# Performance work log

Hardware: AMD Instinct MI355X
Metric: run time of the kernel (lower is better)

The kernel has to match this reference:

```python
import jax, jax.numpy as jnp
import numpy as np

N_NODES = 100000
N_EDGES = 1600000
D_IN = 128
D_HID = 128
D_OUT = 1


def setup_inputs() -> dict:
    key = jax.random.key(0)
    ks = jax.random.split(key, 8)
    x = jax.random.normal(ks[0], (N_NODES, D_IN), dtype=jnp.float32)
    edge_index = jax.random.randint(ks[1], (2, N_EDGES), 0, N_NODES, dtype=jnp.int64)
    s1 = 1.0 / np.sqrt(D_IN)
    s2 = 1.0 / np.sqrt(D_HID)
    W1 = jax.random.uniform(ks[2], (D_IN, D_HID), jnp.float32, -s1, s1)
    b1 = jnp.zeros((D_HID,), jnp.float32)
    W2 = jax.random.uniform(ks[3], (D_HID, D_HID), jnp.float32, -s2, s2)
    b2 = jnp.zeros((D_HID,), jnp.float32)
    Wl = jax.random.uniform(ks[4], (D_HID, D_OUT), jnp.float32, -s2, s2)
    bl = jax.random.uniform(ks[5], (D_OUT,), jnp.float32, -s2, s2)
    return {"x": x, "edge_index": edge_index, "W1": W1, "b1": b1,
            "W2": W2, "b2": b2, "Wl": Wl, "bl": bl}


def _gcn_norm(edge_index, num_nodes):
    # Add self-loops, compute symmetric normalization 1/sqrt(deg_s * deg_d).
    loops = jnp.arange(num_nodes, dtype=edge_index.dtype)
    src = jnp.concatenate([edge_index[0], loops])
    dst = jnp.concatenate([edge_index[1], loops])
    deg = jax.ops.segment_sum(jnp.ones_like(dst, dtype=jnp.float32), dst,
                              num_segments=num_nodes)
    dinv = jnp.where(deg > 0, jax.lax.rsqrt(deg), 0.0)
    norm = dinv[src] * dinv[dst]  # [E + N]
    return src, dst, norm


def _gcn_conv(h, W, b, src, dst, norm, num_nodes):
    h = h @ W                                  # [N, d_out]
    msg = h[src] * norm[:, None]               # [E+N, d_out] gather
    out = jax.ops.segment_sum(msg, dst, num_segments=num_nodes)  # scatter-add
    return out + b


def reference(x, edge_index, W1, b1, W2, b2, Wl, bl):
    num_nodes = x.shape[0]
    src, dst, norm = _gcn_norm(edge_index, num_nodes)
    h = jax.nn.relu(_gcn_conv(x, W1, b1, src, dst, norm, num_nodes))
    # dropout is identity in eval mode
    h = jax.nn.relu(_gcn_conv(h, W2, b2, src, dst, norm, num_nodes))
    return h @ Wl + bl
```

## Files before the change

### kernel.cpp

```cpp
#include <hip/hip_runtime.h>

#define DHID 128
#define BCAP 10240
#define PCHUNK 4096

typedef _Float16 h4 __attribute__((ext_vector_type(4)));
typedef _Float16 h8 __attribute__((ext_vector_type(8)));
typedef _Float16 f16x8 __attribute__((ext_vector_type(8)));
typedef float    f32x4 __attribute__((ext_vector_type(4)));

__global__ __launch_bounds__(256) void k_partition(const int* __restrict__ ei, int E, int nbuck,
                                                   int* __restrict__ bucket_cursor,
                                                   unsigned* __restrict__ packed) {
    __shared__ unsigned sdata[PCHUNK];
    __shared__ int lcnt[256], lbase[256], loff[256], lcur[256], sscan[256];
    int t = threadIdx.x;
    int e0 = blockIdx.x * PCHUNK;
    lcnt[t] = 0;
    __syncthreads();

    for (int i = t; i < PCHUNK; i += 256) {
        int e = e0 + i;
        if (e < E) {
            int d = ei[E + e];
            atomicAdd(&lcnt[d >> 9], 1);
        }
    }
    __syncthreads();

    int c = lcnt[t];
    sscan[t] = c;
    __syncthreads();
    for (int off = 1; off < 256; off <<= 1) {
        int v = (t >= off) ? sscan[t - off] : 0;
        __syncthreads();
        sscan[t] += v;
        __syncthreads();
    }
    loff[t] = sscan[t] - c;
    if (t < nbuck && c > 0) lbase[t] = atomicAdd(&bucket_cursor[t], c);
    lcur[t] = sscan[t] - c;
    __syncthreads();

    for (int i = t; i < PCHUNK; i += 256) {
        int e = e0 + i;
        if (e < E) {
            int s = ei[e];
            int d = ei[E + e];
            int b = d >> 9;
            int pos = atomicAdd(&lcur[b], 1);
            sdata[pos] = ((unsigned)(d & 511) << 17) | (unsigned)s;
        }
    }
    __syncthreads();

    int wid = t >> 6, lane = t & 63;
    for (int b = wid; b < nbuck; b += 4) {
        int cb = lcnt[b];
        if (cb == 0) continue;
        int gbase = b * BCAP + lbase[b];
        int sbase = loff[b];
        for (int k = lane; k < cb; k += 64) packed[gbase + k] = sdata[sbase + k];
    }
}

__global__ __launch_bounds__(256) void k_p2a(const unsigned* __restrict__ packed,
                                             const int* __restrict__ bucket_cursor,
                                             int* __restrict__ cnt, int N) {
    __shared__ int c512[512];
    int t = threadIdx.x, b = blockIdx.x;
    c512[t] = 0; c512[t + 256] = 0;
    __syncthreads();
    int m = bucket_cursor[b];
    const unsigned* pb = packed + (size_t)b * BCAP;
    for (int i = t; i < m; i += 256) atomicAdd(&c512[pb[i] >> 17], 1);
    __syncthreads();
    int base = b << 9;
#pragma unroll
    for (int j = 0; j < 2; ++j) {
        int node = base + t + j * 256;
        if (node < N) cnt[node] = c512[t + j * 256];
    }
}

__global__ void k_dinv(const int* __restrict__ cnt, float* __restrict__ dinv, int N) {
    int i = blockIdx.x * 256 + threadIdx.x;
    if (i < N) dinv[i] = rsqrtf((float)(cnt[i] + 1));
}

__global__ void k_reduce(const int* __restrict__ cnt, int* __restrict__ partial, int N) {
    __shared__ int s[256];
    int t = threadIdx.x;
    int i = blockIdx.x * 256 + t;
    s[t] = (i < N) ? cnt[i] : 0;
    __syncthreads();
    for (int st = 128; st > 0; st >>= 1) {
        if (t < st) s[t] += s[t + st];
        __syncthreads();
    }
    if (t == 0) partial[blockIdx.x] = s[0];
}

__global__ void k_scan_partials(const int* __restrict__ partial, int* __restrict__ blockoff, int NB) {
    __shared__ int s[1024];
    int t = threadIdx.x;
    s[t] = (t < NB) ? partial[t] : 0;
    __syncthreads();
    for (int off = 1; off < 1024; off <<= 1) {
        int v = (t >= off) ? s[t - off] : 0;
        __syncthreads();
        s[t] += v;
        __syncthreads();
    }
    if (t < NB) blockoff[t] = (t == 0) ? 0 : s[t - 1];
}

__global__ void k_scan_block(const int* __restrict__ cnt, const int* __restrict__ blockoff,
                             int* __restrict__ row_ptr, int N, int E) {
    __shared__ int s[256];
    int t = threadIdx.x;
    int i = blockIdx.x * 256 + t;
    int c = (i < N) ? cnt[i] : 0;
    s[t] = c;
    __syncthreads();
    for (int off = 1; off < 256; off <<= 1) {
        int v = (t >= off) ? s[t - off] : 0;
        __syncthreads();
        s[t] += v;
        __syncthreads();
    }
    if (i < N) row_ptr[i] = blockoff[blockIdx.x] + s[t] - c;
    if (i == 0) row_ptr[N] = E;
}

__global__ __launch_bounds__(256) void k_p2b(const unsigned* __restrict__ packed,
                                             const int* __restrict__ bucket_cursor,
                                             const int* __restrict__ row_ptr,
                                             int* __restrict__ csr, int N) {
    __shared__ int c512[512], cur512[512], sscan[256];
    int t = threadIdx.x, b = blockIdx.x;
    c512[t] = 0; c512[t + 256] = 0;
    __syncthreads();
    int m = bucket_cursor[b];
    const unsigned* pb = packed + (size_t)b * BCAP;
    for (int i = t; i < m; i += 256) atomicAdd(&c512[pb[i] >> 17], 1);
    __syncthreads();
    int v0 = c512[2 * t], v1 = c512[2 * t + 1];
    int ps = v0 + v1;
    sscan[t] = ps;
    __syncthreads();
    for (int off = 1; off < 256; off <<= 1) {
        int v = (t >= off) ? sscan[t - off] : 0;
        __syncthreads();
        sscan[t] += v;
        __syncthreads();
    }
    int excl = sscan[t] - ps;
    cur512[2 * t] = excl;
    cur512[2 * t + 1] = excl + v0;
    __syncthreads();
    int rbase = row_ptr[b << 9];
    for (int i = t; i < m; i += 256) {
        unsigned p = pb[i];
        int dl = p >> 17;
        int src = (int)(p & 0x1FFFFu);
        int pos = atomicAdd(&cur512[dl], 1);
        csr[rbase + pos] = src;
    }
}

template <typename TIN>
__global__ __launch_bounds__(256) void k_gemm_mfma(const TIN* __restrict__ X,
                                                   const float* __restrict__ W,
                                                   const float* __restrict__ dinv,
                                                   _Float16* __restrict__ Th,
                                                   int N, int nRB) {
    int t = threadIdx.x;
    int w = t >> 6;
    int l = t & 63;
    int l16 = l & 15;
    int lq = l >> 4;

    f16x8 afrag[2][4];
#pragma unroll
    for (int ct = 0; ct < 2; ++ct) {
        int c = w * 32 + ct * 16 + l16;
#pragma unroll
        for (int kb = 0; kb < 4; ++kb) {
            f16x8 a;
#pragma unroll
            for (int j = 0; j < 8; ++j)
                a[j] = (_Float16)W[(kb * 32 + lq * 8 + j) * DHID + c];
            afrag[ct][kb] = a;
        }
    }

    for (int rb = blockIdx.x; rb < nRB; rb += gridDim.x) {
        int r0 = rb * 32;
        f16x8 bfrag[2][4];
#pragma unroll
        for (int rt = 0; rt < 2; ++rt) {
            int r = r0 + rt * 16 + l16;
            int rc = (r < N) ? r : N - 1;
            const TIN* xp = X + (size_t)rc * DHID + lq * 8;
#pragma unroll
            for (int kb = 0; kb < 4; ++kb) {
                if constexpr (sizeof(TIN) == 4) {
                    float4 x0 = *(const float4*)((const float*)xp + kb * 32);
                    float4 x1 = *(const float4*)((const float*)xp + kb * 32 + 4);
                    f16x8 b;
                    b[0] = (_Float16)x0.x; b[1] = (_Float16)x0.y;
                    b[2] = (_Float16)x0.z; b[3] = (_Float16)x0.w;
                    b[4] = (_Float16)x1.x; b[5] = (_Float16)x1.y;
                    b[6] = (_Float16)x1.z; b[7] = (_Float16)x1.w;
                    bfrag[rt][kb] = b;
                } else {
                    bfrag[rt][kb] = *(const f16x8*)((const _Float16*)xp + kb * 32);
                }
            }
        }

        f32x4 acc[2][2];
#pragma unroll
        for (int rt = 0; rt < 2; ++rt)
#pragma unroll
            for (int ct = 0; ct < 2; ++ct) {
                f32x4 d = {0.f, 0.f, 0.f, 0.f};
#pragma unroll
                for (int kb = 0; kb < 4; ++kb)
                    d = __builtin_amdgcn_mfma_f32_16x16x32_f16(afrag[ct][kb], bfrag[rt][kb], d, 0, 0, 0);
                acc[rt][ct] = d;
            }

#pragma unroll
        for (int rt = 0; rt < 2; ++rt) {
            int r = r0 + rt * 16 + l16;
            if (r < N) {
                float s = dinv[r];
#pragma unroll
                for (int ct = 0; ct < 2; ++ct) {
                    h4 v;
#pragma unroll
                    for (int j = 0; j < 4; ++j) v[j] = (_Float16)(acc[rt][ct][j] * s);
                    *(h4*)(Th + (size_t)r * DHID + w * 32 + ct * 16 + lq * 4) = v;
                }
            }
        }
    }
}

template <int FINAL>
__global__ __launch_bounds__(256) void k_agg(const _Float16* __restrict__ Th,
                                             const int* __restrict__ row_ptr,
                                             const int* __restrict__ csr_src,
                                             const float* __restrict__ dinv,
                                             const float* __restrict__ bias,
                                             void* __restrict__ outp,
                                             const float* __restrict__ Wl,
                                             const float* __restrict__ bl, int N) {
    int node = blockIdx.x * 16 + (threadIdx.x >> 4);
    int sl = threadIdx.x & 15;
    if (node >= N) return;

    int e = row_ptr[node];
    int end = row_ptr[node + 1];
    const h8* Tl = (const h8*)Th + sl;

    float acc[8];
#pragma unroll
    for (int c = 0; c < 8; ++c) acc[c] = 0.f;

    for (; e + 4 <= end; e += 4) {
        int s0 = csr_src[e];
        int s1 = csr_src[e + 1];
        int s2 = csr_src[e + 2];
        int s3 = csr_src[e + 3];
        h8 v0 = Tl[(size_t)s0 * 16];
        h8 v1 = Tl[(size_t)s1 * 16];
        h8 v2 = Tl[(size_t)s2 * 16];
        h8 v3 = Tl[(size_t)s3 * 16];
#pragma unroll
        for (int c = 0; c < 8; ++c)
            acc[c] += ((float)v0[c] + (float)v1[c]) + ((float)v2[c] + (float)v3[c]);
    }
    for (; e < end; ++e) {
        int s0 = csr_src[e];
        h8 va = Tl[(size_t)s0 * 16];
#pragma unroll
        for (int c = 0; c < 8; ++c) acc[c] += (float)va[c];
    }

    {
        h8 tv = Tl[(size_t)node * 16];
#pragma unroll
        for (int c = 0; c < 8; ++c) acc[c] += (float)tv[c];
    }

    float dn = dinv[node];
    const float* bp = bias + sl * 8;
    float4 b0 = *(const float4*)bp;
    float4 b1 = *(const float4*)(bp + 4);
    float r[8];
    r[0] = fmaxf(fmaf(dn, acc[0], b0.x), 0.f);
    r[1] = fmaxf(fmaf(dn, acc[1], b0.y), 0.f);
    r[2] = fmaxf(fmaf(dn, acc[2], b0.z), 0.f);
    r[3] = fmaxf(fmaf(dn, acc[3], b0.w), 0.f);
    r[4] = fmaxf(fmaf(dn, acc[4], b1.x), 0.f);
    r[5] = fmaxf(fmaf(dn, acc[5], b1.y), 0.f);
    r[6] = fmaxf(fmaf(dn, acc[6], b1.z), 0.f);
    r[7] = fmaxf(fmaf(dn, acc[7], b1.w), 0.f);

    if (FINAL == 0) {
        h8 v;
#pragma unroll
        for (int c = 0; c < 8; ++c) v[c] = (_Float16)r[c];
        *(h8*)((_Float16*)outp + (size_t)node * DHID + sl * 8) = v;
    } else {
        const float* wp = Wl + sl * 8;
        float4 w0 = *(const float4*)wp;
        float4 w1 = *(const float4*)(wp + 4);
        float p = r[0] * w0.x + r[1] * w0.y + r[2] * w0.z + r[3] * w0.w +
                  r[4] * w1.x + r[5] * w1.y + r[6] * w1.z + r[7] * w1.w;
#pragma unroll
        for (int off = 8; off > 0; off >>= 1) p += __shfl_down(p, off, 16);
        if (sl == 0) ((float*)outp)[node] = p + bl[0];
    }
}

extern "C" void kernel_launch(void* const* d_in, const int* in_sizes, int n_in,
                              void* d_out, int out_size, void* d_ws, size_t ws_size,
                              hipStream_t stream) {
    const float* x  = (const float*)d_in[0];
    const int*   ei = (const int*)d_in[1];
    const float* W1 = (const float*)d_in[2];
    const float* b1 = (const float*)d_in[3];
    const float* W2 = (const float*)d_in[4];
    const float* b2 = (const float*)d_in[5];
    const float* Wl = (const float*)d_in[6];
    const float* bl = (const float*)d_in[7];
    float* out = (float*)d_out;

    int N = in_sizes[0] / DHID;
    int E = in_sizes[1] / 2;
    int NB = (N + 255) / 256;
    int nbuck = (N + 511) / 512;
    int nRB = (N + 31) / 32;

    char* ws = (char*)d_ws;
    size_t off = 0;
    auto alloc = [&](size_t bytes) -> void* {
        void* p = ws + off;
        off += (bytes + 255) & ~(size_t)255;
        return p;
    };
    int*      cnt      = (int*)alloc((size_t)N * 4);
    float*    dinv     = (float*)alloc((size_t)N * 4);
    int*      row_ptr  = (int*)alloc((size_t)(N + 1) * 4);
    int*      partial  = (int*)alloc((size_t)NB * 4);
    int*      blockoff = (int*)alloc((size_t)NB * 4);
    int*      bcur     = (int*)alloc((size_t)nbuck * 4);
    int*      csr      = (int*)alloc((size_t)E * 4);
    unsigned* packed   = (unsigned*)alloc((size_t)nbuck * BCAP * 4);
    _Float16* Th       = (_Float16*)alloc((size_t)N * DHID * 2);
    _Float16* H        = (_Float16*)alloc((size_t)N * DHID * 2);

    (void)hipMemsetAsync(bcur, 0, (size_t)nbuck * 4, stream);
    k_partition<<<(E + PCHUNK - 1) / PCHUNK, 256, 0, stream>>>(ei, E, nbuck, bcur, packed);
    k_p2a<<<nbuck, 256, 0, stream>>>(packed, bcur, cnt, N);
    k_dinv<<<NB, 256, 0, stream>>>(cnt, dinv, N);
    k_reduce<<<NB, 256, 0, stream>>>(cnt, partial, N);
    k_scan_partials<<<1, 1024, 0, stream>>>(partial, blockoff, NB);
    k_scan_block<<<NB, 256, 0, stream>>>(cnt, blockoff, row_ptr, N, E);
    k_p2b<<<nbuck, 256, 0, stream>>>(packed, bcur, row_ptr, csr, N);

    k_gemm_mfma<float><<<1024, 256, 0, stream>>>(x, W1, dinv, Th, N, nRB);
    k_agg<0><<<(N + 15) / 16, 256, 0, stream>>>(Th, row_ptr, csr, dinv, b1, H, nullptr, nullptr, N);

    k_gemm_mfma<_Float16><<<1024, 256, 0, stream>>>(H, W2, dinv, Th, N, nRB);
    k_agg<1><<<(N + 15) / 16, 256, 0, stream>>>(Th, row_ptr, csr, dinv, b2, out, Wl, bl, N);
}
```

Measured before the change: 245.3 us.

## Stage GEMM input tiles in LDS and split aggregation into feature slices

The GEMM kernel now loads 64-row tiles of X into padded shared memory with coalesced row loads, then feeds MFMA from LDS, processing four row tiles per block iteration. Aggregation is split into 8 feature slices of 16 columns per block, so each gather reads 4 bytes per lane and an L2 holds a slice's working set better. The final layer writes per-slice partial dot products that a new reduce kernel sums. The cost is 8x more reads of the CSR index and row pointers, plus an extra launch and a partial buffer.

```diff
diff --git a/kernel.cpp b/kernel.cpp
--- a/kernel.cpp
+++ b/kernel.cpp
@@ -3,7 +3,9 @@
 #define DHID 128
 #define BCAP 10240
 #define PCHUNK 4096
-
+#define XS_LD 136
+
+typedef _Float16 h2 __attribute__((ext_vector_type(2)));
 typedef _Float16 h4 __attribute__((ext_vector_type(4)));
 typedef _Float16 h8 __attribute__((ext_vector_type(8)));
 typedef _Float16 f16x8 __attribute__((ext_vector_type(8)));
@@ -175,6 +177,7 @@
                                                    const float* __restrict__ dinv,
                                                    _Float16* __restrict__ Th,
                                                    int N, int nRB) {
+    __shared__ _Float16 Xs[64 * XS_LD];
     int t = threadIdx.x;
     int w = t >> 6;
     int l = t & 63;
@@ -195,45 +198,56 @@
         }
     }
 
+    int rs = t >> 2;
+    int cs = (t & 3) * 32;
+
     for (int rb = blockIdx.x; rb < nRB; rb += gridDim.x) {
-        int r0 = rb * 32;
-        f16x8 bfrag[2][4];
-#pragma unroll
-        for (int rt = 0; rt < 2; ++rt) {
-            int r = r0 + rt * 16 + l16;
-            int rc = (r < N) ? r : N - 1;
-            const TIN* xp = X + (size_t)rc * DHID + lq * 8;
+        int r0 = rb * 64;
+        {
+            int rg = r0 + rs; if (rg > N - 1) rg = N - 1;
+            _Float16* sp = Xs + rs * XS_LD + cs;
+            if constexpr (sizeof(TIN) == 4) {
+                const float* xp = (const float*)X + (size_t)rg * DHID + cs;
+#pragma unroll
+                for (int k = 0; k < 4; ++k) {
+                    float4 a = *(const float4*)(xp + k * 8);
+                    float4 b = *(const float4*)(xp + k * 8 + 4);
+                    h8 v;
+                    v[0] = (_Float16)a.x; v[1] = (_Float16)a.y;
+                    v[2] = (_Float16)a.z; v[3] = (_Float16)a.w;
+                    v[4] = (_Float16)b.x; v[5] = (_Float16)b.y;
+                    v[6] = (_Float16)b.z; v[7] = (_Float16)b.w;
+                    *(h8*)(sp + k * 8) = v;
+                }
+            } else {
+                const _Float16* xp = (const _Float16*)X + (size_t)rg * DHID + cs;
+#pragma unroll
+                for (int k = 0; k < 4; ++k)
+                    *(h8*)(sp + k * 8) = *(const h8*)(xp + k * 8);
+            }
+        }
+        __syncthreads();
+
+        f32x4 acc[4][2];
+#pragma unroll
+        for (int rt = 0; rt < 4; ++rt)
+#pragma unroll
+            for (int ct = 0; ct < 2; ++ct) acc[rt][ct] = (f32x4){0.f, 0.f, 0.f, 0.f};
+
+#pragma unroll
+        for (int rt = 0; rt < 4; ++rt) {
+            const _Float16* bp = Xs + (rt * 16 + l16) * XS_LD + lq * 8;
 #pragma unroll
             for (int kb = 0; kb < 4; ++kb) {
-                if constexpr (sizeof(TIN) == 4) {
-                    float4 x0 = *(const float4*)((const float*)xp + kb * 32);
-                    float4 x1 = *(const float4*)((const float*)xp + kb * 32 + 4);
-                    f16x8 b;
-                    b[0] = (_Float16)x0.x; b[1] = (_Float16)x0.y;
-                    b[2] = (_Float16)x0.z; b[3] = (_Float16)x0.w;
-                    b[4] = (_Float16)x1.x; b[5] = (_Float16)x1.y;
-                    b[6] = (_Float16)x1.z; b[7] = (_Float16)x1.w;
-                    bfrag[rt][kb] = b;
-                } else {
-                    bfrag[rt][kb] = *(const f16x8*)((const _Float16*)xp + kb * 32);
-                }
+                f16x8 b = *(const f16x8*)(bp + kb * 32);
+                acc[rt][0] = __builtin_amdgcn_mfma_f32_16x16x32_f16(afrag[0][kb], b, acc[rt][0], 0, 0, 0);
+                acc[rt][1] = __builtin_amdgcn_mfma_f32_16x16x32_f16(afrag[1][kb], b, acc[rt][1], 0, 0, 0);
             }
         }
-
-        f32x4 acc[2][2];
-#pragma unroll
-        for (int rt = 0; rt < 2; ++rt)
-#pragma unroll
-            for (int ct = 0; ct < 2; ++ct) {
-                f32x4 d = {0.f, 0.f, 0.f, 0.f};
-#pragma unroll
-                for (int kb = 0; kb < 4; ++kb)
-                    d = __builtin_amdgcn_mfma_f32_16x16x32_f16(afrag[ct][kb], bfrag[rt][kb], d, 0, 0, 0);
-                acc[rt][ct] = d;
-            }
-
-#pragma unroll
-        for (int rt = 0; rt < 2; ++rt) {
+        __syncthreads();
+
+#pragma unroll
+        for (int rt = 0; rt < 4; ++rt) {
             int r = r0 + rt * 16 + l16;
             if (r < N) {
                 float s = dinv[r];
@@ -250,80 +264,77 @@
 }
 
 template <int FINAL>
-__global__ __launch_bounds__(256) void k_agg(const _Float16* __restrict__ Th,
-                                             const int* __restrict__ row_ptr,
-                                             const int* __restrict__ csr_src,
-                                             const float* __restrict__ dinv,
-                                             const float* __restrict__ bias,
-                                             void* __restrict__ outp,
-                                             const float* __restrict__ Wl,
-                                             const float* __restrict__ bl, int N) {
-    int node = blockIdx.x * 16 + (threadIdx.x >> 4);
-    int sl = threadIdx.x & 15;
+__global__ __launch_bounds__(256) void k_agg_slice(const _Float16* __restrict__ Th,
+                                                   const int* __restrict__ row_ptr,
+                                                   const int* __restrict__ csr_src,
+                                                   const float* __restrict__ dinv,
+                                                   const float* __restrict__ bias,
+                                                   _Float16* __restrict__ H,
+                                                   const float* __restrict__ Wl,
+                                                   float* __restrict__ Ppart, int N) {
+    int slice = blockIdx.x & 7;
+    int chunk = blockIdx.x >> 3;
+    int g  = threadIdx.x >> 3;
+    int l8 = threadIdx.x & 7;
+    int node = chunk * 32 + g;
     if (node >= N) return;
 
     int e = row_ptr[node];
     int end = row_ptr[node + 1];
-    const h8* Tl = (const h8*)Th + sl;
-
-    float acc[8];
-#pragma unroll
-    for (int c = 0; c < 8; ++c) acc[c] = 0.f;
-
+    const h2* Tl = (const h2*)Th + slice * 8 + l8;
+
+    float ax = 0.f, ay = 0.f;
     for (; e + 4 <= end; e += 4) {
         int s0 = csr_src[e];
         int s1 = csr_src[e + 1];
         int s2 = csr_src[e + 2];
         int s3 = csr_src[e + 3];
-        h8 v0 = Tl[(size_t)s0 * 16];
-        h8 v1 = Tl[(size_t)s1 * 16];
-        h8 v2 = Tl[(size_t)s2 * 16];
-        h8 v3 = Tl[(size_t)s3 * 16];
-#pragma unroll
-        for (int c = 0; c < 8; ++c)
-            acc[c] += ((float)v0[c] + (float)v1[c]) + ((float)v2[c] + (float)v3[c]);
+        h2 v0 = Tl[(size_t)s0 * 64];
+        h2 v1 = Tl[(size_t)s1 * 64];
+        h2 v2 = Tl[(size_t)s2 * 64];
+        h2 v3 = Tl[(size_t)s3 * 64];
+        ax += ((float)v0.x + (float)v1.x) + ((float)v2.x + (float)v3.x);
+        ay += ((float)v0.y + (float)v1.y) + ((float)v2.y + (float)v3.y);
     }
     for (; e < end; ++e) {
         int s0 = csr_src[e];
-        h8 va = Tl[(size_t)s0 * 16];
-#pragma unroll
-        for (int c = 0; c < 8; ++c) acc[c] += (float)va[c];
+        h2 v = Tl[(size_t)s0 * 64];
+        ax += (float)v.x;
+        ay += (float)v.y;
     }
 
     {
-        h8 tv = Tl[(size_t)node * 16];
-#pragma unroll
-        for (int c = 0; c < 8; ++c) acc[c] += (float)tv[c];
+        h2 tv = Tl[(size_t)node * 64];
+        ax += (float)tv.x;
+        ay += (float)tv.y;
     }
 
     float dn = dinv[node];
-    const float* bp = bias + sl * 8;
-    float4 b0 = *(const float4*)bp;
-    float4 b1 = *(const float4*)(bp + 4);
-    float r[8];
-    r[0] = fmaxf(fmaf(dn, acc[0], b0.x), 0.f);
-    r[1] = fmaxf(fmaf(dn, acc[1], b0.y), 0.f);
-    r[2] = fmaxf(fmaf(dn, acc[2], b0.z), 0.f);
-    r[3] = fmaxf(fmaf(dn, acc[3], b0.w), 0.f);
-    r[4] = fmaxf(fmaf(dn, acc[4], b1.x), 0.f);
-    r[5] = fmaxf(fmaf(dn, acc[5], b1.y), 0.f);
-    r[6] = fmaxf(fmaf(dn, acc[6], b1.z), 0.f);
-    r[7] = fmaxf(fmaf(dn, acc[7], b1.w), 0.f);
+    float2 b = *(const float2*)(bias + slice * 16 + l8 * 2);
+    float r0 = fmaxf(fmaf(dn, ax, b.x), 0.f);
+    float r1 = fmaxf(fmaf(dn, ay, b.y), 0.f);
 
     if (FINAL == 0) {
-        h8 v;
-#pragma unroll
-        for (int c = 0; c < 8; ++c) v[c] = (_Float16)r[c];
-        *(h8*)((_Float16*)outp + (size_t)node * DHID + sl * 8) = v;
+        h2 v; v.x = (_Float16)r0; v.y = (_Float16)r1;
+        *(h2*)(H + (size_t)node * DHID + slice * 16 + l8 * 2) = v;
     } else {
-        const float* wp = Wl + sl * 8;
-        float4 w0 = *(const float4*)wp;
-        float4 w1 = *(const float4*)(wp + 4);
-        float p = r[0] * w0.x + r[1] * w0.y + r[2] * w0.z + r[3] * w0.w +
-                  r[4] * w1.x + r[5] * w1.y + r[6] * w1.z + r[7] * w1.w;
-#pragma unroll
-        for (int off = 8; off > 0; off >>= 1) p += __shfl_down(p, off, 16);
-        if (sl == 0) ((float*)outp)[node] = p + bl[0];
+        float2 wl = *(const float2*)(Wl + slice * 16 + l8 * 2);
+        float p = fmaf(r0, wl.x, r1 * wl.y);
+        p += __shfl_down(p, 4, 8);
+        p += __shfl_down(p, 2, 8);
+        p += __shfl_down(p, 1, 8);
+        if (l8 == 0) Ppart[(size_t)slice * N + node] = p;
+    }
+}
+
+__global__ void k_out_reduce(const float* __restrict__ Ppart, const float* __restrict__ bl,
+                             float* __restrict__ out, int N) {
+    int i = blockIdx.x * 256 + threadIdx.x;
+    if (i < N) {
+        float s = bl[0];
+#pragma unroll
+        for (int k = 0; k < 8; ++k) s += Ppart[(size_t)k * N + i];
+        out[i] = s;
     }
 }
 
@@ -344,7 +355,8 @@
     int E = in_sizes[1] / 2;
     int NB = (N + 255) / 256;
     int nbuck = (N + 511) / 512;
-    int nRB = (N + 31) / 32;
+    int nRB = (N + 63) / 64;
+    int nchunk = (N + 31) / 32;
 
     char* ws = (char*)d_ws;
     size_t off = 0;
@@ -363,6 +375,7 @@
     unsigned* packed   = (unsigned*)alloc((size_t)nbuck * BCAP * 4);
     _Float16* Th       = (_Float16*)alloc((size_t)N * DHID * 2);
     _Float16* H        = (_Float16*)alloc((size_t)N * DHID * 2);
+    float*    Ppart    = (float*)alloc((size_t)8 * N * 4);
 
     (void)hipMemsetAsync(bcur, 0, (size_t)nbuck * 4, stream);
     k_partition<<<(E + PCHUNK - 1) / PCHUNK, 256, 0, stream>>>(ei, E, nbuck, bcur, packed);
@@ -374,8 +387,9 @@
     k_p2b<<<nbuck, 256, 0, stream>>>(packed, bcur, row_ptr, csr, N);
 
     k_gemm_mfma<float><<<1024, 256, 0, stream>>>(x, W1, dinv, Th, N, nRB);
-    k_agg<0><<<(N + 15) / 16, 256, 0, stream>>>(Th, row_ptr, csr, dinv, b1, H, nullptr, nullptr, N);
+    k_agg_slice<0><<<nchunk * 8, 256, 0, stream>>>(Th, row_ptr, csr, dinv, b1, H, nullptr, nullptr, N);
 
     k_gemm_mfma<_Float16><<<1024, 256, 0, stream>>>(H, W2, dinv, Th, N, nRB);
-    k_agg<1><<<(N + 15) / 16, 256, 0, stream>>>(Th, row_ptr, csr, dinv, b2, out, Wl, bl, N);
-}
+    k_agg_slice<1><<<nchunk * 8, 256, 0, stream>>>(Th, row_ptr, csr, dinv, b2, nullptr, Wl, Ppart, N);
+    k_out_reduce<<<NB, 256, 0, stream>>>(Ppart, bl, out, N);
+}
```

After: 485.6 us. 1.98x slower.

## Stage X tile in LDS for MFMA GEMM and fold dinv into count kernel

Applied to the files above, without the earlier changes.

The GEMM kernel drops its persistent grid-stride loop of 32-row blocks. It now launches one block per 64 rows, loads the tile coalesced into padded shared memory and has each wave read B fragments from LDS. Previously every wave reloaded the same X rows from global memory, and this change is meant to remove those redundant reads. Separately, the dinv computation is fused into k_p2a, which removes one kernel launch. The cost is re-reading the W fragments per block, since the grid is no longer persistent, and more blocks with an LDS footprint.

```diff
diff --git a/kernel.cpp b/kernel.cpp
--- a/kernel.cpp
+++ b/kernel.cpp
@@ -3,6 +3,7 @@
 #define DHID 128
 #define BCAP 10240
 #define PCHUNK 4096
+#define XS_LD 136
 
 typedef _Float16 h4 __attribute__((ext_vector_type(4)));
 typedef _Float16 h8 __attribute__((ext_vector_type(8)));
@@ -66,7 +67,8 @@
 
 __global__ __launch_bounds__(256) void k_p2a(const unsigned* __restrict__ packed,
                                              const int* __restrict__ bucket_cursor,
-                                             int* __restrict__ cnt, int N) {
+                                             int* __restrict__ cnt,
+                                             float* __restrict__ dinv, int N) {
     __shared__ int c512[512];
     int t = threadIdx.x, b = blockIdx.x;
     c512[t] = 0; c512[t + 256] = 0;
@@ -79,13 +81,12 @@
 #pragma unroll
     for (int j = 0; j < 2; ++j) {
         int node = base + t + j * 256;
-        if (node < N) cnt[node] = c512[t + j * 256];
-    }
-}
-
-__global__ void k_dinv(const int* __restrict__ cnt, float* __restrict__ dinv, int N) {
-    int i = blockIdx.x * 256 + threadIdx.x;
-    if (i < N) dinv[i] = rsqrtf((float)(cnt[i] + 1));
+        if (node < N) {
+            int c = c512[t + j * 256];
+            cnt[node] = c;
+            dinv[node] = rsqrtf((float)(c + 1));
+        }
+    }
 }
 
 __global__ void k_reduce(const int* __restrict__ cnt, int* __restrict__ partial, int N) {
@@ -173,8 +174,8 @@
 __global__ __launch_bounds__(256) void k_gemm_mfma(const TIN* __restrict__ X,
                                                    const float* __restrict__ W,
                                                    const float* __restrict__ dinv,
-                                                   _Float16* __restrict__ Th,
-                                                   int N, int nRB) {
+                                                   _Float16* __restrict__ Th, int N) {
+    __shared__ _Float16 Xs[64 * XS_LD];
     int t = threadIdx.x;
     int w = t >> 6;
     int l = t & 63;
@@ -195,55 +196,63 @@
         }
     }
 
-    for (int rb = blockIdx.x; rb < nRB; rb += gridDim.x) {
-        int r0 = rb * 32;
-        f16x8 bfrag[2][4];
-#pragma unroll
-        for (int rt = 0; rt < 2; ++rt) {
-            int r = r0 + rt * 16 + l16;
-            int rc = (r < N) ? r : N - 1;
-            const TIN* xp = X + (size_t)rc * DHID + lq * 8;
-#pragma unroll
-            for (int kb = 0; kb < 4; ++kb) {
-                if constexpr (sizeof(TIN) == 4) {
-                    float4 x0 = *(const float4*)((const float*)xp + kb * 32);
-                    float4 x1 = *(const float4*)((const float*)xp + kb * 32 + 4);
-                    f16x8 b;
-                    b[0] = (_Float16)x0.x; b[1] = (_Float16)x0.y;
-                    b[2] = (_Float16)x0.z; b[3] = (_Float16)x0.w;
-                    b[4] = (_Float16)x1.x; b[5] = (_Float16)x1.y;
-                    b[6] = (_Float16)x1.z; b[7] = (_Float16)x1.w;
-                    bfrag[rt][kb] = b;
-                } else {
-                    bfrag[rt][kb] = *(const f16x8*)((const _Float16*)xp + kb * 32);
-                }
+    int rs = t >> 2;
+    int cs = (t & 3) * 32;
+
+    int r0 = blockIdx.x * 64;
+    {
+        int rg = r0 + rs; if (rg > N - 1) rg = N - 1;
+        _Float16* sp = Xs + rs * XS_LD + cs;
+        if constexpr (sizeof(TIN) == 4) {
+            const float* xp = (const float*)X + (size_t)rg * DHID + cs;
+#pragma unroll
+            for (int k = 0; k < 4; ++k) {
+                float4 a = *(const float4*)(xp + k * 8);
+                float4 b = *(const float4*)(xp + k * 8 + 4);
+                h8 v;
+                v[0] = (_Float16)a.x; v[1] = (_Float16)a.y;
+                v[2] = (_Float16)a.z; v[3] = (_Float16)a.w;
+                v[4] = (_Float16)b.x; v[5] = (_Float16)b.y;
+                v[6] = (_Float16)b.z; v[7] = (_Float16)b.w;
+                *(h8*)(sp + k * 8) = v;
             }
-        }
-
-        f32x4 acc[2][2];
-#pragma unroll
-        for (int rt = 0; rt < 2; ++rt)
+        } else {
+            const _Float16* xp = (const _Float16*)X + (size_t)rg * DHID + cs;
+#pragma unroll
+            for (int k = 0; k < 4; ++k)
+                *(h8*)(sp + k * 8) = *(const h8*)(xp + k * 8);
+        }
+    }
+    __syncthreads();
+
+    f32x4 acc[4][2];
+#pragma unroll
+    for (int rt = 0; rt < 4; ++rt)
+#pragma unroll
+        for (int ct = 0; ct < 2; ++ct) acc[rt][ct] = (f32x4){0.f, 0.f, 0.f, 0.f};
+
+#pragma unroll
+    for (int rt = 0; rt < 4; ++rt) {
+        const _Float16* bp = Xs + (rt * 16 + l16) * XS_LD + lq * 8;
+#pragma unroll
+        for (int kb = 0; kb < 4; ++kb) {
+            f16x8 b = *(const f16x8*)(bp + kb * 32);
+            acc[rt][0] = __builtin_amdgcn_mfma_f32_16x16x32_f16(afrag[0][kb], b, acc[rt][0], 0, 0, 0);
+            acc[rt][1] = __builtin_amdgcn_mfma_f32_16x16x32_f16(afrag[1][kb], b, acc[rt][1], 0, 0, 0);
+        }
+    }
+
+#pragma unroll
+    for (int rt = 0; rt < 4; ++rt) {
+        int r = r0 + rt * 16 + l16;
+        if (r < N) {
+            float s = dinv[r];
 #pragma unroll
             for (int ct = 0; ct < 2; ++ct) {
-                f32x4 d = {0.f, 0.f, 0.f, 0.f};
-#pragma unroll
-                for (int kb = 0; kb < 4; ++kb)
-                    d = __builtin_amdgcn_mfma_f32_16x16x32_f16(afrag[ct][kb], bfrag[rt][kb], d, 0, 0, 0);
-                acc[rt][ct] = d;
-            }
-
-#pragma unroll
-        for (int rt = 0; rt < 2; ++rt) {
-            int r = r0 + rt * 16 + l16;
-            if (r < N) {
-                float s = dinv[r];
-#pragma unroll
-                for (int ct = 0; ct < 2; ++ct) {
-                    h4 v;
-#pragma unroll
-                    for (int j = 0; j < 4; ++j) v[j] = (_Float16)(acc[rt][ct][j] * s);
-                    *(h4*)(Th + (size_t)r * DHID + w * 32 + ct * 16 + lq * 4) = v;
-                }
+                h4 v;
+#pragma unroll
+                for (int j = 0; j < 4; ++j) v[j] = (_Float16)(acc[rt][ct][j] * s);
+                *(h4*)(Th + (size_t)r * DHID + w * 32 + ct * 16 + lq * 4) = v;
             }
         }
     }
@@ -344,7 +353,7 @@
     int E = in_sizes[1] / 2;
     int NB = (N + 255) / 256;
     int nbuck = (N + 511) / 512;
-    int nRB = (N + 31) / 32;
+    int nRB = (N + 63) / 64;
 
     char* ws = (char*)d_ws;
     size_t off = 0;
@@ -366,16 +375,15 @@
 
     (void)hipMemsetAsync(bcur, 0, (size_t)nbuck * 4, stream);
     k_partition<<<(E + PCHUNK - 1) / PCHUNK, 256, 0, stream>>>(ei, E, nbuck, bcur, packed);
-    k_p2a<<<nbuck, 256, 0, stream>>>(packed, bcur, cnt, N);
-    k_dinv<<<NB, 256, 0, stream>>>(cnt, dinv, N);
+    k_p2a<<<nbuck, 256, 0, stream>>>(packed, bcur, cnt, dinv, N);
     k_reduce<<<NB, 256, 0, stream>>>(cnt, partial, N);
     k_scan_partials<<<1, 1024, 0, stream>>>(partial, blockoff, NB);
     k_scan_block<<<NB, 256, 0, stream>>>(cnt, blockoff, row_ptr, N, E);
     k_p2b<<<nbuck, 256, 0, stream>>>(packed, bcur, row_ptr, csr, N);
 
-    k_gemm_mfma<float><<<1024, 256, 0, stream>>>(x, W1, dinv, Th, N, nRB);
+    k_gemm_mfma<float><<<nRB, 256, 0, stream>>>(x, W1, dinv, Th, N);
     k_agg<0><<<(N + 15) / 16, 256, 0, stream>>>(Th, row_ptr, csr, dinv, b1, H, nullptr, nullptr, N);
 
-    k_gemm_mfma<_Float16><<<1024, 256, 0, stream>>>(H, W2, dinv, Th, N, nRB);
+    k_gemm_mfma<_Float16><<<nRB, 256, 0, stream>>>(H, W2, dinv, Th, N);
     k_agg<1><<<(N + 15) / 16, 256, 0, stream>>>(Th, row_ptr, csr, dinv, b2, out, Wl, bl, N);
 }
```

Result: faster. 229.8 us (-6.3%).
